# Optimization experiments

Measured on AMD Instinct MI355X. Metric: run time of the kernel, lower is better.

Reference implementation:

```python
import jax, jax.numpy as jnp
import numpy as np

N, E = 50000, 500000
D_IN, D_HID, D_OUT = 512, 512, 256


def setup_inputs() -> dict:
    key = jax.random.key(0)
    ks = jax.random.split(key, 8)
    x = jax.random.normal(ks[0], (N, D_IN), dtype=jnp.float32)
    edge_index1 = jax.random.randint(ks[1], (2, E), 0, N, dtype=jnp.int64)
    edge_index2 = jax.random.randint(ks[2], (2, E), 0, N, dtype=jnp.int64)
    s_in = 1.0 / np.sqrt(D_IN)
    s_hid = 1.0 / np.sqrt(D_HID)
    W1l = jax.random.normal(ks[3], (D_HID, D_IN), dtype=jnp.float32) * s_in
    W1r = jax.random.normal(ks[4], (D_HID, D_IN), dtype=jnp.float32) * s_in
    b1 = jnp.zeros((D_HID,), dtype=jnp.float32)
    W2l = jax.random.normal(ks[5], (D_OUT, D_HID), dtype=jnp.float32) * s_hid
    W2r = jax.random.normal(ks[6], (D_OUT, D_HID), dtype=jnp.float32) * s_hid
    b2 = jnp.zeros((D_OUT,), dtype=jnp.float32)
    return {"x": x, "edge_index1": edge_index1, "edge_index2": edge_index2,
            "W1l": W1l, "b1": b1, "W1r": W1r, "W2l": W2l, "b2": b2, "W2r": W2r}


def _sage_conv(x_src, x_dst, edge_index, Wl, b, Wr):
    # PyG SAGEConv (aggr='mean', root_weight=True): lin_l(mean_agg) + lin_r(x_dst)
    src, dst = edge_index[0], edge_index[1]
    n_dst = x_dst.shape[0]
    msgs = x_src[src]                                        # [E, d] gather
    agg = jax.ops.segment_sum(msgs, dst, num_segments=n_dst)  # [n_dst, d]
    deg = jax.ops.segment_sum(jnp.ones((src.shape[0],), x_src.dtype), dst,
                              num_segments=n_dst)
    agg = agg / jnp.maximum(deg, 1.0)[:, None]                # mean
    return agg @ Wl.T + b + x_dst @ Wr.T


def reference(x, edge_index1, edge_index2, W1l, b1, W1r, W2l, b2, W2r):
    # layer 1 (+ relu; dropout is identity in eval mode)
    h = _sage_conv(x, x, edge_index1, W1l, b1, W1r)
    h = jax.nn.relu(h)
    # layer 2
    h = _sage_conv(h, h, edge_index2, W2l, b2, W2r)
    return jax.nn.log_softmax(h, axis=-1)
```

## Files before the change

### kernel.cpp

```cpp
#include <hip/hip_runtime.h>
#include <math.h>

#define DIN  512
#define DHID 512
#define DOUT 256

typedef __attribute__((ext_vector_type(8))) short short8;
typedef __attribute__((ext_vector_type(4))) float f32x4;
typedef __attribute__((ext_vector_type(2))) float floatx2;

__device__ __forceinline__ unsigned short f2bf(float f) {
    unsigned int u = __float_as_uint(f);
    u += 0x7fffu + ((u >> 16) & 1u);
    return (unsigned short)(u >> 16);
}
__device__ __forceinline__ float bflo(unsigned int w) { return __uint_as_float(w << 16); }
__device__ __forceinline__ float bfhi(unsigned int w) { return __uint_as_float(w & 0xffff0000u); }

__device__ __forceinline__ void cvt8(const float* __restrict__ in,
                                     unsigned short* __restrict__ out, int i) {
    const float4* iv = (const float4*)in;
    float4 a = iv[2 * i], b = iv[2 * i + 1];
    uint4 o;
    o.x = (unsigned)f2bf(a.x) | ((unsigned)f2bf(a.y) << 16);
    o.y = (unsigned)f2bf(a.z) | ((unsigned)f2bf(a.w) << 16);
    o.z = (unsigned)f2bf(b.x) | ((unsigned)f2bf(b.y) << 16);
    o.w = (unsigned)f2bf(b.z) | ((unsigned)f2bf(b.w) << 16);
    ((uint4*)out)[i] = o;
}

__global__ void k_f2bf(const float* __restrict__ in, unsigned short* __restrict__ out, int n8) {
    int i = blockIdx.x * blockDim.x + threadIdx.x;
    if (i < n8) cvt8(in, out, i);
}

__global__ void k_wcvt(const float* __restrict__ W1l, const float* __restrict__ W1r,
                       const float* __restrict__ W2l, const float* __restrict__ W2r,
                       unsigned short* __restrict__ w1, unsigned short* __restrict__ w2) {
    int i = blockIdx.x * blockDim.x + threadIdx.x;
    if (i < 32768)        cvt8(W1l, w1, i);
    else if (i < 65536)   cvt8(W1r, w1 + 262144, i - 32768);
    else if (i < 81920)   cvt8(W2l, w2, i - 65536);
    else if (i < 98304)   cvt8(W2r, w2 + 131072, i - 81920);
}

__global__ void k_count2(const int* __restrict__ d1, const int* __restrict__ d2,
                         int* __restrict__ deg1, int* __restrict__ deg2, int E1, int E2) {
    int e = blockIdx.x * blockDim.x + threadIdx.x;
    if (blockIdx.y == 0) { if (e < E1) atomicAdd(&deg1[d1[e]], 1); }
    else                 { if (e < E2) atomicAdd(&deg2[d2[e]], 1); }
}

#define SCAN_B 256
__global__ void k_scan_partial2(const int* __restrict__ deg1, const int* __restrict__ deg2,
                                int* __restrict__ part1, int* __restrict__ part2, int n) {
    __shared__ int s[SCAN_B];
    const int* deg = blockIdx.y ? deg2 : deg1;
    int* part      = blockIdx.y ? part2 : part1;
    int i = blockIdx.x * SCAN_B + threadIdx.x;
    s[threadIdx.x] = (i < n) ? deg[i] : 0;
    __syncthreads();
    for (int off = SCAN_B / 2; off > 0; off >>= 1) {
        if (threadIdx.x < off) s[threadIdx.x] += s[threadIdx.x + off];
        __syncthreads();
    }
    if (threadIdx.x == 0) part[blockIdx.x] = s[0];
}

__global__ void k_scan_part2b(int* __restrict__ part1, int* __restrict__ part2, int nb,
                              int* __restrict__ rowptr1, int* __restrict__ rowptr2, int n) {
    __shared__ int s[SCAN_B];
    int* part   = blockIdx.x ? part2 : part1;
    int* rowptr = blockIdx.x ? rowptr2 : rowptr1;
    int v = (threadIdx.x < nb) ? part[threadIdx.x] : 0;
    s[threadIdx.x] = v;
    __syncthreads();
    for (int off = 1; off < SCAN_B; off <<= 1) {
        int t = (threadIdx.x >= off) ? s[threadIdx.x - off] : 0;
        __syncthreads();
        s[threadIdx.x] += t;
        __syncthreads();
    }
    if (threadIdx.x < nb) part[threadIdx.x] = s[threadIdx.x] - v;
    if (threadIdx.x == SCAN_B - 1) rowptr[n] = s[SCAN_B - 1];
}

__global__ void k_scan_final2(const int* __restrict__ deg1, const int* __restrict__ deg2,
                              const int* __restrict__ part1, const int* __restrict__ part2,
                              int* __restrict__ rowptr1, int* __restrict__ rowptr2,
                              int* __restrict__ cursor1, int* __restrict__ cursor2, int n) {
    __shared__ int s[SCAN_B];
    const int* deg  = blockIdx.y ? deg2 : deg1;
    const int* part = blockIdx.y ? part2 : part1;
    int* rowptr     = blockIdx.y ? rowptr2 : rowptr1;
    int* cursor     = blockIdx.y ? cursor2 : cursor1;
    int i = blockIdx.x * SCAN_B + threadIdx.x;
    int v = (i < n) ? deg[i] : 0;
    s[threadIdx.x] = v;
    __syncthreads();
    for (int off = 1; off < SCAN_B; off <<= 1) {
        int t = (threadIdx.x >= off) ? s[threadIdx.x - off] : 0;
        __syncthreads();
        s[threadIdx.x] += t;
        __syncthreads();
    }
    if (i < n) {
        int ex = part[blockIdx.x] + s[threadIdx.x] - v;
        rowptr[i] = ex;
        cursor[i] = ex;
    }
}

__global__ void k_fill2(const int* __restrict__ s1, const int* __restrict__ d1,
                        const int* __restrict__ s2, const int* __restrict__ d2,
                        int* __restrict__ cur1, int* __restrict__ cur2,
                        int* __restrict__ col1, int* __restrict__ col2, int E1, int E2) {
    int e = blockIdx.x * blockDim.x + threadIdx.x;
    if (blockIdx.y == 0) {
        if (e < E1) { int p = atomicAdd(&cur1[d1[e]], 1); col1[p] = s1[e]; }
    } else {
        if (e < E2) { int p = atomicAdd(&cur2[d2[e]], 1); col2[p] = s2[e]; }
    }
}

#define TM 128
#define TN 128
#define TK 32

template <int NCT, int SPLIT>
__global__ __launch_bounds__(256, 4)
void k_gemm_mfma(const unsigned short* __restrict__ A, const unsigned short* __restrict__ W,
                 unsigned char* __restrict__ C8, unsigned short* __restrict__ C16,
                 int M, int K, int NC) {
    __shared__ __align__(16) unsigned short As[TM * TK];
    __shared__ __align__(16) unsigned short Bs[TN * TK];
    const int id = blockIdx.x;
    const int xcd = id & 7;
    const int s = id >> 3;
    const int row0 = ((s / NCT) * 8 + xcd) * TM;
    const int col0 = (s % NCT) * TN;
    if (row0 >= M) return;

    const int t = threadIdx.x;
    const int lane = t & 63;
    const int w = t >> 6;
    const int wr = (w >> 1) * 64;
    const int wc = (w & 1) * 64;
    const int lm = lane & 15;
    const int q = lane >> 4;

    f32x4 acc[4][4];
#pragma unroll
    for (int i = 0; i < 4; ++i)
#pragma unroll
        for (int j = 0; j < 4; ++j) acc[i][j] = (f32x4){0.f, 0.f, 0.f, 0.f};

    const int ar = t >> 2;
    const int as = (((t & 3) ^ ((t >> 3) & 3))) * 8;

    for (int k0 = 0; k0 < K; k0 += TK) {
        int r1 = row0 + ar;      if (r1 >= M) r1 = M - 1;
        int r2 = row0 + ar + 64; if (r2 >= M) r2 = M - 1;
        const unsigned short* ga1 = A + (size_t)r1 * K + k0 + as;
        const unsigned short* ga2 = A + (size_t)r2 * K + k0 + as;
        const unsigned short* gb1 = W + (size_t)(col0 + ar) * K + k0 + as;
        const unsigned short* gb2 = W + (size_t)(col0 + ar + 64) * K + k0 + as;
        __builtin_amdgcn_global_load_lds(
            (const __attribute__((address_space(1))) unsigned int*)ga1,
            (__attribute__((address_space(3))) unsigned int*)&As[t * 8], 16, 0, 0);
        __builtin_amdgcn_global_load_lds(
            (const __attribute__((address_space(1))) unsigned int*)ga2,
            (__attribute__((address_space(3))) unsigned int*)&As[(t + 256) * 8], 16, 0, 0);
        __builtin_amdgcn_global_load_lds(
            (const __attribute__((address_space(1))) unsigned int*)gb1,
            (__attribute__((address_space(3))) unsigned int*)&Bs[t * 8], 16, 0, 0);
        __builtin_amdgcn_global_load_lds(
            (const __attribute__((address_space(1))) unsigned int*)gb2,
            (__attribute__((address_space(3))) unsigned int*)&Bs[(t + 256) * 8], 16, 0, 0);
        __syncthreads();

        short8 a[4], b[4];
#pragma unroll
        for (int i = 0; i < 4; ++i) {
            int R = wr + i * 16 + lm;
            a[i] = *(const short8*)&As[R * TK + ((q ^ ((R >> 1) & 3)) * 8)];
        }
#pragma unroll
        for (int j = 0; j < 4; ++j) {
            int R = wc + j * 16 + lm;
            b[j] = *(const short8*)&Bs[R * TK + ((q ^ ((R >> 1) & 3)) * 8)];
        }
#pragma unroll
        for (int i = 0; i < 4; ++i)
#pragma unroll
            for (int j = 0; j < 4; ++j)
                acc[i][j] = __builtin_amdgcn_mfma_f32_16x16x32_bf16(a[i], b[j], acc[i][j], 0, 0, 0);
        __syncthreads();
    }

    const int qr = (lane >> 4) * 4;
    const bool lo_half = SPLIT && (col0 < NC / 2);
    const int cadj = SPLIT ? NC / 2 : 0;
#pragma unroll
    for (int i = 0; i < 4; ++i) {
#pragma unroll
        for (int r = 0; r < 4; ++r) {
            int gr = row0 + wr + i * 16 + qr + r;
            if (gr >= M) continue;
#pragma unroll
            for (int j = 0; j < 4; ++j) {
                int gc = col0 + wc + j * 16 + lm;
                float v = acc[i][j][r];
                if (SPLIT && lo_half) {
                    int p = __builtin_amdgcn_cvt_pk_fp8_f32(v, v, 0, 0);
                    C8[(size_t)gr * (NC / 2) + gc] = (unsigned char)p;
                } else {
                    C16[(size_t)gr * (NC - cadj) + (gc - cadj)] = f2bf(v);
                }
            }
        }
    }
}

__global__ void k_agg_relu(const unsigned char* __restrict__ C8,
                           const unsigned short* __restrict__ C16r,
                           const int* __restrict__ rowptr, const int* __restrict__ col,
                           const float* __restrict__ b1, unsigned short* __restrict__ H, int n) {
    int node = blockIdx.x * (blockDim.x >> 6) + (threadIdx.x >> 6);
    int lane = threadIdx.x & 63;
    if (node >= n) return;
    int beg = rowptr[node], end = rowptr[node + 1];
    float acc[8] = {};
    const uint2* Cv = (const uint2*)C8;
    int e = beg;
    for (; e + 4 <= end; e += 4) {
        int c0 = col[e], c1 = col[e + 1], c2 = col[e + 2], c3 = col[e + 3];
        uint2 v0 = Cv[(size_t)c0 * 64 + lane];
        uint2 v1 = Cv[(size_t)c1 * 64 + lane];
        uint2 v2 = Cv[(size_t)c2 * 64 + lane];
        uint2 v3 = Cv[(size_t)c3 * 64 + lane];
        unsigned int ws[8] = {v0.x, v0.y, v1.x, v1.y, v2.x, v2.y, v3.x, v3.y};
#pragma unroll
        for (int qq = 0; qq < 8; ++qq) {
            floatx2 flo = __builtin_amdgcn_cvt_pk_f32_fp8(ws[qq], 0);
            floatx2 fhi = __builtin_amdgcn_cvt_pk_f32_fp8(ws[qq], 1);
            int base = (qq & 1) * 4;
            acc[base + 0] += flo.x; acc[base + 1] += flo.y;
            acc[base + 2] += fhi.x; acc[base + 3] += fhi.y;
        }
    }
    for (; e < end; ++e) {
        uint2 v = Cv[(size_t)col[e] * 64 + lane];
        floatx2 f0 = __builtin_amdgcn_cvt_pk_f32_fp8(v.x, 0);
        floatx2 f1 = __builtin_amdgcn_cvt_pk_f32_fp8(v.x, 1);
        floatx2 f2 = __builtin_amdgcn_cvt_pk_f32_fp8(v.y, 0);
        floatx2 f3 = __builtin_amdgcn_cvt_pk_f32_fp8(v.y, 1);
        acc[0] += f0.x; acc[1] += f0.y; acc[2] += f1.x; acc[3] += f1.y;
        acc[4] += f2.x; acc[5] += f2.y; acc[6] += f3.x; acc[7] += f3.y;
    }
    float inv = 1.0f / fmaxf((float)(end - beg), 1.0f);
    uint4 yr = ((const uint4*)C16r)[(size_t)node * 64 + lane];
    unsigned int wr[4] = {yr.x, yr.y, yr.z, yr.w};
    float4 bv0 = ((const float4*)b1)[2 * lane];
    float4 bv1 = ((const float4*)b1)[2 * lane + 1];
    float bb[8] = {bv0.x, bv0.y, bv0.z, bv0.w, bv1.x, bv1.y, bv1.z, bv1.w};
    unsigned int r[4];
#pragma unroll
    for (int qq = 0; qq < 4; ++qq) {
        float v0 = fmaxf(acc[2 * qq] * inv     + bflo(wr[qq]) + bb[2 * qq],     0.f);
        float v1 = fmaxf(acc[2 * qq + 1] * inv + bfhi(wr[qq]) + bb[2 * qq + 1], 0.f);
        r[qq] = (unsigned)f2bf(v0) | ((unsigned)f2bf(v1) << 16);
    }
    uint4 o; o.x = r[0]; o.y = r[1]; o.z = r[2]; o.w = r[3];
    ((uint4*)H)[(size_t)node * 64 + lane] = o;
}

__global__ void k_agg_lsm(const unsigned char* __restrict__ C8,
                          const unsigned short* __restrict__ C16r,
                          const int* __restrict__ rowptr, const int* __restrict__ col,
                          const float* __restrict__ b2, float* __restrict__ O, int n) {
    int node = blockIdx.x * (blockDim.x >> 6) + (threadIdx.x >> 6);
    int lane = threadIdx.x & 63;
    if (node >= n) return;
    int beg = rowptr[node], end = rowptr[node + 1];
    float acc[4] = {};
    const unsigned int* Cv = (const unsigned int*)C8;
    int e = beg;
    for (; e + 4 <= end; e += 4) {
        int c0 = col[e], c1 = col[e + 1], c2 = col[e + 2], c3 = col[e + 3];
        unsigned int u0 = Cv[(size_t)c0 * 64 + lane];
        unsigned int u1 = Cv[(size_t)c1 * 64 + lane];
        unsigned int u2 = Cv[(size_t)c2 * 64 + lane];
        unsigned int u3 = Cv[(size_t)c3 * 64 + lane];
        unsigned int us[4] = {u0, u1, u2, u3};
#pragma unroll
        for (int qq = 0; qq < 4; ++qq) {
            floatx2 flo = __builtin_amdgcn_cvt_pk_f32_fp8(us[qq], 0);
            floatx2 fhi = __builtin_amdgcn_cvt_pk_f32_fp8(us[qq], 1);
            acc[0] += flo.x; acc[1] += flo.y; acc[2] += fhi.x; acc[3] += fhi.y;
        }
    }
    for (; e < end; ++e) {
        unsigned int u = Cv[(size_t)col[e] * 64 + lane];
        floatx2 flo = __builtin_amdgcn_cvt_pk_f32_fp8(u, 0);
        floatx2 fhi = __builtin_amdgcn_cvt_pk_f32_fp8(u, 1);
        acc[0] += flo.x; acc[1] += flo.y; acc[2] += fhi.x; acc[3] += fhi.y;
    }
    float inv = 1.0f / fmaxf((float)(end - beg), 1.0f);
    uint2 yr = ((const uint2*)C16r)[(size_t)node * 64 + lane];
    float4 bv = ((const float4*)b2)[lane];
    float val[4];
    val[0] = acc[0] * inv + bflo(yr.x) + bv.x;
    val[1] = acc[1] * inv + bfhi(yr.x) + bv.y;
    val[2] = acc[2] * inv + bflo(yr.y) + bv.z;
    val[3] = acc[3] * inv + bfhi(yr.y) + bv.w;
    float mx = fmaxf(fmaxf(val[0], val[1]), fmaxf(val[2], val[3]));
#pragma unroll
    for (int off = 32; off > 0; off >>= 1) mx = fmaxf(mx, __shfl_xor(mx, off));
    float s = expf(val[0] - mx) + expf(val[1] - mx) + expf(val[2] - mx) + expf(val[3] - mx);
#pragma unroll
    for (int off = 32; off > 0; off >>= 1) s += __shfl_xor(s, off);
    float lse = mx + logf(s);
    float4 o = make_float4(val[0] - lse, val[1] - lse, val[2] - lse, val[3] - lse);
    ((float4*)O)[(size_t)node * 64 + lane] = o;
}

extern "C" void kernel_launch(void* const* d_in, const int* in_sizes, int n_in,
                              void* d_out, int out_size, void* d_ws, size_t ws_size,
                              hipStream_t stream) {
    const float* x   = (const float*)d_in[0];
    const int*   ei1 = (const int*)d_in[1];
    const int*   ei2 = (const int*)d_in[2];
    const float* W1l = (const float*)d_in[3];
    const float* b1  = (const float*)d_in[4];
    const float* W1r = (const float*)d_in[5];
    const float* W2l = (const float*)d_in[6];
    const float* b2  = (const float*)d_in[7];
    const float* W2r = (const float*)d_in[8];
    float* out = (float*)d_out;

    const int N  = in_sizes[0] / DIN;
    const int E1 = in_sizes[1] / 2;
    const int E2 = in_sizes[2] / 2;
    const int Emax = (E1 > E2) ? E1 : E2;
    const int NB = (N + SCAN_B - 1) / SCAN_B;

    unsigned short* x_bf  = (unsigned short*)d_ws;
    unsigned short* h_bf  = x_bf + (size_t)N * 512;
    unsigned char*  c1l   = (unsigned char*)(h_bf + (size_t)N * 512);
    unsigned short* c1r   = (unsigned short*)(c1l + (size_t)N * 512);
    unsigned char*  c2l   = c1l;
    unsigned short* c2r   = (unsigned short*)(c2l + (size_t)N * 256);
    unsigned short* w1_bf = c1r + (size_t)N * 512;
    unsigned short* w2_bf = w1_bf + 1024 * 512;
    int* rowptr1 = (int*)(w2_bf + 512 * 512);
    int* rowptr2 = rowptr1 + (N + 1);
    int* cursor1 = rowptr2 + (N + 1);
    int* cursor2 = cursor1 + N;
    int* deg1    = cursor2 + N;
    int* deg2    = deg1 + N;
    int* part1   = deg2 + N;
    int* part2   = part1 + 256;
    int* col1    = part2 + 256;
    int* col2    = col1 + E1;
    (void)ws_size; (void)n_in; (void)out_size;

    {
        int n8 = N * 512 / 8;
        k_f2bf<<<(n8 + 255) / 256, 256, 0, stream>>>(x, x_bf, n8);
        k_wcvt<<<(98304 + 255) / 256, 256, 0, stream>>>(W1l, W1r, W2l, W2r, w1_bf, w2_bf);
    }

    hipMemsetAsync(deg1, 0, (size_t)2 * N * sizeof(int), stream);
    {
        dim3 ge((Emax + 255) / 256, 2);
        k_count2<<<ge, 256, 0, stream>>>(ei1 + E1, ei2 + E2, deg1, deg2, E1, E2);
        k_scan_partial2<<<dim3(NB, 2), SCAN_B, 0, stream>>>(deg1, deg2, part1, part2, N);
        k_scan_part2b<<<2, SCAN_B, 0, stream>>>(part1, part2, NB, rowptr1, rowptr2, N);
        k_scan_final2<<<dim3(NB, 2), SCAN_B, 0, stream>>>(deg1, deg2, part1, part2,
                                                          rowptr1, rowptr2, cursor1, cursor2, N);
        k_fill2<<<ge, 256, 0, stream>>>(ei1, ei1 + E1, ei2, ei2 + E2,
                                        cursor1, cursor2, col1, col2, E1, E2);
    }

    const int MB = (N + TM - 1) / TM;
    const int G8 = (MB + 7) / 8;

    k_gemm_mfma<8, 1><<<G8 * 8 * 8, 256, 0, stream>>>(x_bf, w1_bf, c1l, c1r, N, DIN, 1024);
    k_agg_relu<<<(N + 3) / 4, 256, 0, stream>>>(c1l, c1r, rowptr1, col1, b1, h_bf, N);

    k_gemm_mfma<4, 1><<<G8 * 8 * 4, 256, 0, stream>>>(h_bf, w2_bf, c2l, c2r, N, DHID, 512);
    k_agg_lsm<<<(N + 3) / 4, 256, 0, stream>>>(c2l, c2r, rowptr2, col2, b2, out, N);
}
```

Before: 480.9 us.

## Replace GEMM with 256x256 double-buffered, phase-interleaved MFMA kernel

Replaces the 128x128x32 single-buffered MFMA GEMM with a 256x256x64 tile kernel using 512 threads and double-buffered LDS. The next K-tile's global-to-LDS loads are interleaved with four MFMA quadrants, gated by partial waitcnt and barriers, with raised wave priority during MFMA. The intent is to hide global load latency and raise data reuse per tile. In exchange it uses more LDS and registers, lowers occupancy, and launches fewer blocks, which can leave CUs idle on the tail.

```diff
diff --git a/kernel.cpp b/kernel.cpp
--- a/kernel.cpp
+++ b/kernel.cpp
@@ -123,93 +123,147 @@
     }
 }
 
-#define TM 128
-#define TN 128
-#define TK 32
+#define BM 256
+#define BN 256
+#define BK 64
+#define LDT (BM * BK)
 
 template <int NCT, int SPLIT>
-__global__ __launch_bounds__(256, 4)
-void k_gemm_mfma(const unsigned short* __restrict__ A, const unsigned short* __restrict__ W,
-                 unsigned char* __restrict__ C8, unsigned short* __restrict__ C16,
-                 int M, int K, int NC) {
-    __shared__ __align__(16) unsigned short As[TM * TK];
-    __shared__ __align__(16) unsigned short Bs[TN * TK];
-    const int id = blockIdx.x;
-    const int xcd = id & 7;
-    const int s = id >> 3;
-    const int row0 = ((s / NCT) * 8 + xcd) * TM;
-    const int col0 = (s % NCT) * TN;
-    if (row0 >= M) return;
+__global__ __launch_bounds__(512, 2)
+void k_gemm_8ph(const unsigned short* __restrict__ A, const unsigned short* __restrict__ W,
+                unsigned char* __restrict__ C8, unsigned short* __restrict__ C16,
+                int M, int K, int NC) {
+    __shared__ __align__(16) unsigned short As[2 * LDT];
+    __shared__ __align__(16) unsigned short Bs[2 * LDT];
+
+    const int id = blockIdx.x, nwg = gridDim.x;
+    const int sid = ((nwg & 7) == 0) ? ((id & 7) * (nwg >> 3) + (id >> 3)) : id;
+    const int row0 = (sid / NCT) * BM;
+    const int col0 = (sid % NCT) * BN;
 
     const int t = threadIdx.x;
     const int lane = t & 63;
     const int w = t >> 6;
-    const int wr = (w >> 1) * 64;
-    const int wc = (w & 1) * 64;
+    const int wm = w >> 2;
+    const int wn = w & 3;
     const int lm = lane & 15;
-    const int q = lane >> 4;
-
-    f32x4 acc[4][4];
-#pragma unroll
-    for (int i = 0; i < 4; ++i)
+    const int lq = lane >> 4;
+    const int l7 = lm & 7;
+    const int cx0 = (lq ^ l7) * 8;
+    const int cx1 = ((4 + lq) ^ l7) * 8;
+
+    const int rl = t >> 3;
+    const int cs = t & 7;
+    const int rB = ((rl >> 5) << 6) + (rl & 31);
+    const int kx = (cs ^ (rl & 7)) * 8;
+
+    const int rA00 = rl,       rA01 = rl + 128;
+    const int rA10 = rl + 64,  rA11 = rl + 192;
+    const int rB00 = rB,       rB01 = rB + 128;
+    const int rB10 = rB + 32,  rB11 = rB + 160;
+
+    #define CLAMPR(r) (((row0 + (r)) < M) ? (row0 + (r)) : (M - 1))
+    const unsigned short* sA00 = A + (size_t)CLAMPR(rA00) * K + kx;
+    const unsigned short* sA01 = A + (size_t)CLAMPR(rA01) * K + kx;
+    const unsigned short* sA10 = A + (size_t)CLAMPR(rA10) * K + kx;
+    const unsigned short* sA11 = A + (size_t)CLAMPR(rA11) * K + kx;
+    const unsigned short* sB00 = W + (size_t)(col0 + rB00) * K + kx;
+    const unsigned short* sB01 = W + (size_t)(col0 + rB01) * K + kx;
+    const unsigned short* sB10 = W + (size_t)(col0 + rB10) * K + kx;
+    const unsigned short* sB11 = W + (size_t)(col0 + rB11) * K + kx;
+
+    const int dA = rl * BK + cs * 8;
+    const int dA00 = dA,            dA01 = dA + 128 * BK;
+    const int dA10 = dA + 64 * BK,  dA11 = dA + 192 * BK;
+    const int dB = rB * BK + cs * 8;
+    const int dB00 = dB,            dB01 = dB + 128 * BK;
+    const int dB10 = dB + 32 * BK,  dB11 = dB + 160 * BK;
+
+    #define GL(SRC, ARR, D) __builtin_amdgcn_global_load_lds( \
+        (const __attribute__((address_space(1))) unsigned int*)(SRC), \
+        (__attribute__((address_space(3))) unsigned int*)&ARR[D], 16, 0, 0)
+
+    f32x4 acc[8][4];
+#pragma unroll
+    for (int i = 0; i < 8; ++i)
 #pragma unroll
         for (int j = 0; j < 4; ++j) acc[i][j] = (f32x4){0.f, 0.f, 0.f, 0.f};
 
-    const int ar = t >> 2;
-    const int as = (((t & 3) ^ ((t >> 3) & 3))) * 8;
-
-    for (int k0 = 0; k0 < K; k0 += TK) {
-        int r1 = row0 + ar;      if (r1 >= M) r1 = M - 1;
-        int r2 = row0 + ar + 64; if (r2 >= M) r2 = M - 1;
-        const unsigned short* ga1 = A + (size_t)r1 * K + k0 + as;
-        const unsigned short* ga2 = A + (size_t)r2 * K + k0 + as;
-        const unsigned short* gb1 = W + (size_t)(col0 + ar) * K + k0 + as;
-        const unsigned short* gb2 = W + (size_t)(col0 + ar + 64) * K + k0 + as;
-        __builtin_amdgcn_global_load_lds(
-            (const __attribute__((address_space(1))) unsigned int*)ga1,
-            (__attribute__((address_space(3))) unsigned int*)&As[t * 8], 16, 0, 0);
-        __builtin_amdgcn_global_load_lds(
-            (const __attribute__((address_space(1))) unsigned int*)ga2,
-            (__attribute__((address_space(3))) unsigned int*)&As[(t + 256) * 8], 16, 0, 0);
-        __builtin_amdgcn_global_load_lds(
-            (const __attribute__((address_space(1))) unsigned int*)gb1,
-            (__attribute__((address_space(3))) unsigned int*)&Bs[t * 8], 16, 0, 0);
-        __builtin_amdgcn_global_load_lds(
-            (const __attribute__((address_space(1))) unsigned int*)gb2,
-            (__attribute__((address_space(3))) unsigned int*)&Bs[(t + 256) * 8], 16, 0, 0);
-        __syncthreads();
-
-        short8 a[4], b[4];
-#pragma unroll
-        for (int i = 0; i < 4; ++i) {
-            int R = wr + i * 16 + lm;
-            a[i] = *(const short8*)&As[R * TK + ((q ^ ((R >> 1) & 3)) * 8)];
-        }
-#pragma unroll
-        for (int j = 0; j < 4; ++j) {
-            int R = wc + j * 16 + lm;
-            b[j] = *(const short8*)&Bs[R * TK + ((q ^ ((R >> 1) & 3)) * 8)];
-        }
-#pragma unroll
-        for (int i = 0; i < 4; ++i)
-#pragma unroll
-            for (int j = 0; j < 4; ++j)
-                acc[i][j] = __builtin_amdgcn_mfma_f32_16x16x32_bf16(a[i], b[j], acc[i][j], 0, 0, 0);
-        __syncthreads();
-    }
-
-    const int qr = (lane >> 4) * 4;
+    GL(sA00, As, dA00); GL(sA01, As, dA01);
+    GL(sA10, As, dA10); GL(sA11, As, dA11);
+    GL(sB00, Bs, dB00); GL(sB01, Bs, dB01);
+    GL(sB10, Bs, dB10); GL(sB11, Bs, dB11);
+
+    short8 af[4][2], bf[2][2];
+
+    #define LOAD_A(mh) do { \
+        const unsigned short* _p = Asb + (wm * 128 + (mh) * 64 + lm) * BK; \
+        _Pragma("unroll") \
+        for (int ii = 0; ii < 4; ++ii) { \
+            af[ii][0] = *(const short8*)(_p + ii * 16 * BK + cx0); \
+            af[ii][1] = *(const short8*)(_p + ii * 16 * BK + cx1); \
+        } } while (0)
+
+    #define LOAD_B(nh) do { \
+        const unsigned short* _p = Bsb + (wn * 64 + (nh) * 32 + lm) * BK; \
+        _Pragma("unroll") \
+        for (int jj = 0; jj < 2; ++jj) { \
+            bf[jj][0] = *(const short8*)(_p + jj * 16 * BK + cx0); \
+            bf[jj][1] = *(const short8*)(_p + jj * 16 * BK + cx1); \
+        } } while (0)
+
+    #define MFMA_Q(mh, nh) do { \
+        __builtin_amdgcn_s_setprio(1); \
+        _Pragma("unroll") \
+        for (int ii = 0; ii < 4; ++ii) \
+        _Pragma("unroll") \
+        for (int jj = 0; jj < 2; ++jj) { \
+            acc[(mh)*4+ii][(nh)*2+jj] = __builtin_amdgcn_mfma_f32_16x16x32_bf16( \
+                af[ii][0], bf[jj][0], acc[(mh)*4+ii][(nh)*2+jj], 0, 0, 0); \
+            acc[(mh)*4+ii][(nh)*2+jj] = __builtin_amdgcn_mfma_f32_16x16x32_bf16( \
+                af[ii][1], bf[jj][1], acc[(mh)*4+ii][(nh)*2+jj], 0, 0, 0); \
+        } \
+        __builtin_amdgcn_s_setprio(0); } while (0)
+
+    const int NT = K / BK;
+    for (int kt = 0; kt < NT; ++kt) {
+        const int bc = (kt & 1) * LDT;
+        const int bb = bc ^ LDT;
+        const unsigned short* Asb = As + bc;
+        const unsigned short* Bsb = Bs + bc;
+        const int ko = ((kt + 1 < NT) ? (kt + 1) : kt) * BK;
+
+        asm volatile("s_waitcnt vmcnt(2) lgkmcnt(0)" ::: "memory");
+        __builtin_amdgcn_s_barrier();
+        LOAD_A(0); LOAD_B(0);
+        GL(sA00 + ko, As, bb + dA00); GL(sA01 + ko, As, bb + dA01);
+        MFMA_Q(0, 0);
+        LOAD_A(1);
+        GL(sA10 + ko, As, bb + dA10); GL(sA11 + ko, As, bb + dA11);
+        MFMA_Q(1, 0);
+        asm volatile("s_waitcnt vmcnt(4) lgkmcnt(0)" ::: "memory");
+        __builtin_amdgcn_s_barrier();
+        LOAD_B(1);
+        GL(sB00 + ko, Bs, bb + dB00); GL(sB01 + ko, Bs, bb + dB01);
+        MFMA_Q(1, 1);
+        LOAD_A(0);
+        GL(sB10 + ko, Bs, bb + dB10); GL(sB11 + ko, Bs, bb + dB11);
+        MFMA_Q(0, 1);
+    }
+    asm volatile("s_waitcnt vmcnt(0)" ::: "memory");
+
+    const int qr = lq * 4;
     const bool lo_half = SPLIT && (col0 < NC / 2);
     const int cadj = SPLIT ? NC / 2 : 0;
 #pragma unroll
-    for (int i = 0; i < 4; ++i) {
+    for (int i = 0; i < 8; ++i) {
 #pragma unroll
         for (int r = 0; r < 4; ++r) {
-            int gr = row0 + wr + i * 16 + qr + r;
+            int gr = row0 + wm * 128 + i * 16 + qr + r;
             if (gr >= M) continue;
 #pragma unroll
             for (int j = 0; j < 4; ++j) {
-                int gc = col0 + wc + j * 16 + lm;
+                int gc = col0 + wn * 64 + j * 16 + lm;
                 float v = acc[i][j][r];
                 if (SPLIT && lo_half) {
                     int p = __builtin_amdgcn_cvt_pk_fp8_f32(v, v, 0, 0);
@@ -220,6 +274,11 @@
             }
         }
     }
+    #undef LOAD_A
+    #undef LOAD_B
+    #undef MFMA_Q
+    #undef GL
+    #undef CLAMPR
 }
 
 __global__ void k_agg_relu(const unsigned char* __restrict__ C8,
@@ -383,12 +442,11 @@
                                         cursor1, cursor2, col1, col2, E1, E2);
     }
 
-    const int MB = (N + TM - 1) / TM;
-    const int G8 = (MB + 7) / 8;
-
-    k_gemm_mfma<8, 1><<<G8 * 8 * 8, 256, 0, stream>>>(x_bf, w1_bf, c1l, c1r, N, DIN, 1024);
+    const int RT = (N + BM - 1) / BM;
+
+    k_gemm_8ph<4, 1><<<RT * 4, 512, 0, stream>>>(x_bf, w1_bf, c1l, c1r, N, DIN, 1024);
     k_agg_relu<<<(N + 3) / 4, 256, 0, stream>>>(c1l, c1r, rowptr1, col1, b1, h_bf, N);
 
-    k_gemm_mfma<4, 1><<<G8 * 8 * 4, 256, 0, stream>>>(h_bf, w2_bf, c2l, c2r, N, DHID, 512);
+    k_gemm_8ph<2, 1><<<RT * 2, 512, 0, stream>>>(h_bf, w2_bf, c2l, c2r, N, DHID, 512);
     k_agg_lsm<<<(N + 3) / 4, 256, 0, stream>>>(c2l, c2r, rowptr2, col2, b2, out, N);
 }
```

After: 517.5 us. 1.08x slower.

## Fuse conversion with degree count and interleave CSR fill into layer-1 GEMM

Applied to the files above, without the earlier changes.

Merges the x and weight bf16 conversion kernels with the degree-counting kernel into one launch. It also removes the separate CSR fill kernel by spreading fill blocks across the layer-1 GEMM grid, so the atomic scatter overlaps the MFMA work. This cuts launch overhead and hides the latency-bound fill behind compute. The GEMM kernel body is duplicated, and fill blocks compete with GEMM blocks for CU slots. The GEMM tile-to-XCD mapping now relies on the remapped block id, which could hurt L2 locality.

```diff
diff --git a/kernel.cpp b/kernel.cpp
--- a/kernel.cpp
+++ b/kernel.cpp
@@ -29,26 +29,24 @@
     ((uint4*)out)[i] = o;
 }
 
-__global__ void k_f2bf(const float* __restrict__ in, unsigned short* __restrict__ out, int n8) {
+__global__ void k_prep_cnt(const float* __restrict__ x, unsigned short* __restrict__ x_bf,
+                           const float* __restrict__ W1l, const float* __restrict__ W1r,
+                           const float* __restrict__ W2l, const float* __restrict__ W2r,
+                           unsigned short* __restrict__ w1, unsigned short* __restrict__ w2,
+                           const int* __restrict__ d1, const int* __restrict__ d2,
+                           int* __restrict__ deg1, int* __restrict__ deg2,
+                           int n8, int E1, int E2, int EB) {
     int i = blockIdx.x * blockDim.x + threadIdx.x;
-    if (i < n8) cvt8(in, out, i);
-}
-
-__global__ void k_wcvt(const float* __restrict__ W1l, const float* __restrict__ W1r,
-                       const float* __restrict__ W2l, const float* __restrict__ W2r,
-                       unsigned short* __restrict__ w1, unsigned short* __restrict__ w2) {
-    int i = blockIdx.x * blockDim.x + threadIdx.x;
-    if (i < 32768)        cvt8(W1l, w1, i);
-    else if (i < 65536)   cvt8(W1r, w1 + 262144, i - 32768);
-    else if (i < 81920)   cvt8(W2l, w2, i - 65536);
-    else if (i < 98304)   cvt8(W2r, w2 + 131072, i - 81920);
-}
-
-__global__ void k_count2(const int* __restrict__ d1, const int* __restrict__ d2,
-                         int* __restrict__ deg1, int* __restrict__ deg2, int E1, int E2) {
-    int e = blockIdx.x * blockDim.x + threadIdx.x;
-    if (blockIdx.y == 0) { if (e < E1) atomicAdd(&deg1[d1[e]], 1); }
-    else                 { if (e < E2) atomicAdd(&deg2[d2[e]], 1); }
+    if (i < n8) { cvt8(x, x_bf, i); return; }
+    i -= n8;
+    if (i < 32768)  { cvt8(W1l, w1, i); return; }
+    if (i < 65536)  { cvt8(W1r, w1 + 262144, i - 32768); return; }
+    if (i < 81920)  { cvt8(W2l, w2, i - 65536); return; }
+    if (i < 98304)  { cvt8(W2r, w2 + 131072, i - 81920); return; }
+    i -= 98304;
+    if (i < EB * 256) { if (i < E1) atomicAdd(&deg1[d1[i]], 1); return; }
+    i -= EB * 256;
+    if (i < E2) atomicAdd(&deg2[d2[i]], 1);
 }
 
 #define SCAN_B 256
@@ -111,21 +109,126 @@
     }
 }
 
-__global__ void k_fill2(const int* __restrict__ s1, const int* __restrict__ d1,
-                        const int* __restrict__ s2, const int* __restrict__ d2,
-                        int* __restrict__ cur1, int* __restrict__ cur2,
-                        int* __restrict__ col1, int* __restrict__ col2, int E1, int E2) {
-    int e = blockIdx.x * blockDim.x + threadIdx.x;
-    if (blockIdx.y == 0) {
-        if (e < E1) { int p = atomicAdd(&cur1[d1[e]], 1); col1[p] = s1[e]; }
-    } else {
-        if (e < E2) { int p = atomicAdd(&cur2[d2[e]], 1); col2[p] = s2[e]; }
-    }
-}
-
 #define TM 128
 #define TN 128
 #define TK 32
+
+template <int NCT, int SPLIT>
+__global__ __launch_bounds__(256, 4)
+void k_gemm_fill(const unsigned short* __restrict__ A, const unsigned short* __restrict__ W,
+                 unsigned char* __restrict__ C8, unsigned short* __restrict__ C16,
+                 int M, int K, int NC, int G, int F,
+                 const int* __restrict__ s1, const int* __restrict__ d1,
+                 const int* __restrict__ s2, const int* __restrict__ d2,
+                 int* __restrict__ cur1, int* __restrict__ cur2,
+                 int* __restrict__ col1, int* __restrict__ col2,
+                 int E1, int E2, int EB) {
+    __shared__ __align__(16) unsigned short As[TM * TK];
+    __shared__ __align__(16) unsigned short Bs[TN * TK];
+
+    const int bid = blockIdx.x;
+    const long long T = (long long)G + F;
+    const int pf = (int)(((long long)bid * F) / T);
+    const bool isFill = (int)(((long long)(bid + 1) * F) / T) > pf;
+    if (isFill) {
+        const int f = pf;
+        if (f < EB) {
+            int e = f * 256 + threadIdx.x;
+            if (e < E1) { int p = atomicAdd(&cur1[d1[e]], 1); col1[p] = s1[e]; }
+        } else {
+            int e = (f - EB) * 256 + threadIdx.x;
+            if (e < E2) { int p = atomicAdd(&cur2[d2[e]], 1); col2[p] = s2[e]; }
+        }
+        return;
+    }
+
+    const int id = bid - pf;
+    const int xcd = id & 7;
+    const int s = id >> 3;
+    const int row0 = ((s / NCT) * 8 + xcd) * TM;
+    const int col0 = (s % NCT) * TN;
+    if (row0 >= M) return;
+
+    const int t = threadIdx.x;
+    const int lane = t & 63;
+    const int w = t >> 6;
+    const int wr = (w >> 1) * 64;
+    const int wc = (w & 1) * 64;
+    const int lm = lane & 15;
+    const int q = lane >> 4;
+
+    f32x4 acc[4][4];
+#pragma unroll
+    for (int i = 0; i < 4; ++i)
+#pragma unroll
+        for (int j = 0; j < 4; ++j) acc[i][j] = (f32x4){0.f, 0.f, 0.f, 0.f};
+
+    const int ar = t >> 2;
+    const int as = (((t & 3) ^ ((t >> 3) & 3))) * 8;
+
+    for (int k0 = 0; k0 < K; k0 += TK) {
+        int r1 = row0 + ar;      if (r1 >= M) r1 = M - 1;
+        int r2 = row0 + ar + 64; if (r2 >= M) r2 = M - 1;
+        const unsigned short* ga1 = A + (size_t)r1 * K + k0 + as;
+        const unsigned short* ga2 = A + (size_t)r2 * K + k0 + as;
+        const unsigned short* gb1 = W + (size_t)(col0 + ar) * K + k0 + as;
+        const unsigned short* gb2 = W + (size_t)(col0 + ar + 64) * K + k0 + as;
+        __builtin_amdgcn_global_load_lds(
+            (const __attribute__((address_space(1))) unsigned int*)ga1,
+            (__attribute__((address_space(3))) unsigned int*)&As[t * 8], 16, 0, 0);
+        __builtin_amdgcn_global_load_lds(
+            (const __attribute__((address_space(1))) unsigned int*)ga2,
+            (__attribute__((address_space(3))) unsigned int*)&As[(t + 256) * 8], 16, 0, 0);
+        __builtin_amdgcn_global_load_lds(
+            (const __attribute__((address_space(1))) unsigned int*)gb1,
+            (__attribute__((address_space(3))) unsigned int*)&Bs[t * 8], 16, 0, 0);
+        __builtin_amdgcn_global_load_lds(
+            (const __attribute__((address_space(1))) unsigned int*)gb2,
+            (__attribute__((address_space(3))) unsigned int*)&Bs[(t + 256) * 8], 16, 0, 0);
+        __syncthreads();
+
+        short8 a[4], b[4];
+#pragma unroll
+        for (int i = 0; i < 4; ++i) {
+            int R = wr + i * 16 + lm;
+            a[i] = *(const short8*)&As[R * TK + ((q ^ ((R >> 1) & 3)) * 8)];
+        }
+#pragma unroll
+        for (int j = 0; j < 4; ++j) {
+            int R = wc + j * 16 + lm;
+            b[j] = *(const short8*)&Bs[R * TK + ((q ^ ((R >> 1) & 3)) * 8)];
+        }
+#pragma unroll
+        for (int i = 0; i < 4; ++i)
+#pragma unroll
+            for (int j = 0; j < 4; ++j)
+                acc[i][j] = __builtin_amdgcn_mfma_f32_16x16x32_bf16(a[i], b[j], acc[i][j], 0, 0, 0);
+        __syncthreads();
+    }
+
+    const int qr = (lane >> 4) * 4;
+    const bool lo_half = SPLIT && (col0 < NC / 2);
+    const int cadj = SPLIT ? NC / 2 : 0;
+#pragma unroll
+    for (int i = 0; i < 4; ++i) {
+#pragma unroll
+        for (int r = 0; r < 4; ++r) {
+            int gr = row0 + wr + i * 16 + qr + r;
+            if (gr >= M) continue;
+#pragma unroll
+            for (int j = 0; j < 4; ++j) {
+                int gc = col0 + wc + j * 16 + lm;
+                float v = acc[i][j][r];
+                if (SPLIT && lo_half) {
+                    int p = __builtin_amdgcn_cvt_pk_fp8_f32(v, v, 0, 0);
+                    C8[(size_t)gr * (NC / 2) + gc] = (unsigned char)p;
+                } else {
+                    C16[(size_t)gr * (NC - cadj) + (gc - cadj)] = f2bf(v);
+                }
+            }
+        }
+    }
+}
 
 template <int NCT, int SPLIT>
 __global__ __launch_bounds__(256, 4)
@@ -344,6 +447,7 @@
     const int E2 = in_sizes[2] / 2;
     const int Emax = (E1 > E2) ? E1 : E2;
     const int NB = (N + SCAN_B - 1) / SCAN_B;
+    const int EB = (Emax + 255) / 256;
 
     unsigned short* x_bf  = (unsigned short*)d_ws;
     unsigned short* h_bf  = x_bf + (size_t)N * 512;
@@ -365,28 +469,29 @@
     int* col2    = col1 + E1;
     (void)ws_size; (void)n_in; (void)out_size;
 
+    hipMemsetAsync(deg1, 0, (size_t)2 * N * sizeof(int), stream);
     {
         int n8 = N * 512 / 8;
-        k_f2bf<<<(n8 + 255) / 256, 256, 0, stream>>>(x, x_bf, n8);
-        k_wcvt<<<(98304 + 255) / 256, 256, 0, stream>>>(W1l, W1r, W2l, W2r, w1_bf, w2_bf);
-    }
-
-    hipMemsetAsync(deg1, 0, (size_t)2 * N * sizeof(int), stream);
-    {
-        dim3 ge((Emax + 255) / 256, 2);
-        k_count2<<<ge, 256, 0, stream>>>(ei1 + E1, ei2 + E2, deg1, deg2, E1, E2);
-        k_scan_partial2<<<dim3(NB, 2), SCAN_B, 0, stream>>>(deg1, deg2, part1, part2, N);
-        k_scan_part2b<<<2, SCAN_B, 0, stream>>>(part1, part2, NB, rowptr1, rowptr2, N);
-        k_scan_final2<<<dim3(NB, 2), SCAN_B, 0, stream>>>(deg1, deg2, part1, part2,
-                                                          rowptr1, rowptr2, cursor1, cursor2, N);
-        k_fill2<<<ge, 256, 0, stream>>>(ei1, ei1 + E1, ei2, ei2 + E2,
-                                        cursor1, cursor2, col1, col2, E1, E2);
-    }
+        int gb = (n8 + 98304 + 255) / 256 + 2 * EB;
+        k_prep_cnt<<<gb, 256, 0, stream>>>(x, x_bf, W1l, W1r, W2l, W2r, w1_bf, w2_bf,
+                                           ei1 + E1, ei2 + E2, deg1, deg2, n8, E1, E2, EB);
+    }
+
+    k_scan_partial2<<<dim3(NB, 2), SCAN_B, 0, stream>>>(deg1, deg2, part1, part2, N);
+    k_scan_part2b<<<2, SCAN_B, 0, stream>>>(part1, part2, NB, rowptr1, rowptr2, N);
+    k_scan_final2<<<dim3(NB, 2), SCAN_B, 0, stream>>>(deg1, deg2, part1, part2,
+                                                      rowptr1, rowptr2, cursor1, cursor2, N);
 
     const int MB = (N + TM - 1) / TM;
     const int G8 = (MB + 7) / 8;
 
-    k_gemm_mfma<8, 1><<<G8 * 8 * 8, 256, 0, stream>>>(x_bf, w1_bf, c1l, c1r, N, DIN, 1024);
+    {
+        const int G = G8 * 8 * 8;
+        const int F = 2 * EB;
+        k_gemm_fill<8, 1><<<G + F, 256, 0, stream>>>(
+            x_bf, w1_bf, c1l, c1r, N, DIN, 1024, G, F,
+            ei1, ei1 + E1, ei2, ei2 + E2, cursor1, cursor2, col1, col2, E1, E2, EB);
+    }
     k_agg_relu<<<(N + 3) / 4, 256, 0, stream>>>(c1l, c1r, rowptr1, col1, b1, h_bf, N);
 
     k_gemm_mfma<4, 1><<<G8 * 8 * 4, 256, 0, stream>>>(h_bf, w2_bf, c2l, c2r, N, DHID, 512);
```

Result: faster. 453.9 us (-5.6%).
